# Performance work log

Hardware: AMD Instinct MI355X
Metric: run time of the kernel (lower is better)

## Reference

```python
import jax, jax.numpy as jnp
import numpy as np

B, C_IN, C, H, W = 32, 2048, 1024, 14, 14
N_CLS = 30


def setup_inputs() -> dict:
    key = jax.random.key(0)
    k1, k2, k3, k4, k5 = jax.random.split(key, 5)
    f1 = jax.random.normal(k1, (B, C_IN, H, W), dtype=jnp.float32)
    f2 = jax.random.normal(k2, (B, C, H, W), dtype=jnp.float32)
    conv_w = jax.random.normal(k3, (C, C_IN), dtype=jnp.float32) * (1.0 / np.sqrt(C_IN))
    fc_w = jax.random.normal(k4, (N_CLS, C), dtype=jnp.float32) * (1.0 / np.sqrt(C))
    fc_b = jax.random.normal(k5, (N_CLS,), dtype=jnp.float32)
    return {"f1": f1, "f2": f2, "conv_w": conv_w, "fc_w": fc_w, "fc_b": fc_b}


def reference(f1, f2, conv_w, fc_w, fc_b):
    # conv1: 1x1 conv 2048 -> 1024, no bias  => channel contraction
    f1c = jnp.einsum('bihw,oi->bohw', f1, conv_w)  # [B, C, H, W]

    # bilinear_pooling: out[b,c,h,i,j] = f1c[b,c,h,i] * f2[b,c,h,j]
    # followed by AdaptiveAvgPool2d((1,1)) over (H, W*W).
    # mean_{h,i,j} f1c*f2 = mean_h[ (mean_i f1c) * (mean_j f2) ]
    xm = jnp.mean(f1c, axis=-1)              # [B, C, H]
    ym = jnp.mean(f2, axis=-1)               # [B, C, H]
    pooled = jnp.mean(xm * ym, axis=-1)      # [B, C]

    # fc head
    return pooled @ fc_w.T + fc_b            # [B, 30]
```

## Files before the change

### kernel.cpp

```cpp
#include <hip/hip_runtime.h>
#include <hip/hip_bf16.h>


typedef __attribute__((ext_vector_type(8))) short short8;
typedef __attribute__((ext_vector_type(4))) float f32x4;

static __device__ __forceinline__ unsigned short f2bf(float f) {
    union { float f; unsigned u; } v; v.f = f;
    return (unsigned short)((v.u + 0x7FFFu + ((v.u >> 16) & 1u)) >> 16);
}

__global__ __launch_bounds__(256) void k1_prep(
    const float* __restrict__ f1, const float* __restrict__ f2,
    const float* __restrict__ cw,
    unsigned short* __restrict__ f1mt, unsigned short* __restrict__ cwb,
    float* __restrict__ ym)
{
    __shared__ float lds[64 * 196];
    const float inv14 = 1.0f / 14.0f;
    int blk = blockIdx.x;
    int tid = threadIdx.x;

    if (blk < 1024) {
        int b = blk >> 5, i0 = (blk & 31) * 64;
        const float4* src = (const float4*)(f1 + (size_t)(b * 2048 + i0) * 196);
        #pragma unroll
        for (int j = 0; j < 13; j++) {
            int idx = j * 256 + tid;
            if (idx < 3136) *(float4*)&lds[idx * 4] = src[idx];
        }
        __syncthreads();
        int r  = tid & 63;
        int hb = tid >> 6;
        unsigned short* o = f1mt + (size_t)b * 16 * 2048 + i0 + r;
        #pragma unroll
        for (int it = 0; it < 4; it++) {
            int h = hb + it * 4;
            if (h < 14) {
                const float* p = &lds[r * 196 + h * 14];
                float s = 0.0f;
                #pragma unroll
                for (int q = 0; q < 14; q++) s += p[q];
                o[h * 2048] = f2bf(s * inv14);
            } else {
                o[h * 2048] = 0;
            }
        }
    } else if (blk < 1536) {
        int t = blk - 1024;
        int b = t >> 4, c0 = (t & 15) * 64;
        const float4* src = (const float4*)(f2 + (size_t)(b * 1024 + c0) * 196);
        #pragma unroll
        for (int j = 0; j < 13; j++) {
            int idx = j * 256 + tid;
            if (idx < 3136) *(float4*)&lds[idx * 4] = src[idx];
        }
        __syncthreads();
        int r  = tid & 63;
        int hb = tid >> 6;
        float* o = ym + (size_t)b * 16 * 1024 + c0 + r;
        #pragma unroll
        for (int it = 0; it < 4; it++) {
            int h = hb + it * 4;
            if (h < 14) {
                const float* p = &lds[r * 196 + h * 14];
                float s = 0.0f;
                #pragma unroll
                for (int q = 0; q < 14; q++) s += p[q];
                o[h * 1024] = s * inv14;
            } else {
                o[h * 1024] = 0.0f;
            }
        }
    } else {
        int t = (blk - 1536) * 256 + tid;
        const float4* p = (const float4*)(cw + (size_t)t * 8);
        float4 v0 = p[0], v1 = p[1];
        ushort4 a, b4;
        a.x = f2bf(v0.x); a.y = f2bf(v0.y); a.z = f2bf(v0.z); a.w = f2bf(v0.w);
        b4.x = f2bf(v1.x); b4.y = f2bf(v1.y); b4.z = f2bf(v1.z); b4.w = f2bf(v1.w);
        *(ushort4*)(cwb + (size_t)t * 8)     = a;
        *(ushort4*)(cwb + (size_t)t * 8 + 4) = b4;
    }
}

__global__ __launch_bounds__(256) void k2_gemm(
    const unsigned short* __restrict__ A,
    const unsigned short* __restrict__ Bm,
    const float* __restrict__ ym,
    float* __restrict__ part)
{
    int tid = threadIdx.x;
    int w  = tid >> 6;
    int l  = tid & 63;
    int lg = l >> 4;
    int lr = l & 15;
    int tile = blockIdx.x >> 2;
    int kq   = blockIdx.x & 3;
    int ct = tile >> 3, nt = tile & 7;
    int c0 = ct * 64, n0 = nt * 64;
    int kc = kq * 4 + w;
    int kbase = kc * 128;

    const unsigned short* Ap = A  + (size_t)(c0 + lr) * 2048 + kbase + lg * 8;
    const unsigned short* Bp = Bm + (size_t)(n0 + lr) * 2048 + kbase + lg * 8;

    short8 af[4][4], bf[4][4];
    #pragma unroll
    for (int mf = 0; mf < 4; mf++)
        #pragma unroll
        for (int kk = 0; kk < 4; kk++)
            af[mf][kk] = *(const short8*)(Ap + mf * 16 * 2048 + kk * 32);
    #pragma unroll
    for (int nf = 0; nf < 4; nf++)
        #pragma unroll
        for (int kk = 0; kk < 4; kk++)
            bf[nf][kk] = *(const short8*)(Bp + nf * 16 * 2048 + kk * 32);

    f32x4 acc[4][4];
    #pragma unroll
    for (int mf = 0; mf < 4; mf++)
        #pragma unroll
        for (int nf = 0; nf < 4; nf++)
            acc[mf][nf] = (f32x4){0.f, 0.f, 0.f, 0.f};

    #pragma unroll
    for (int kk = 0; kk < 4; kk++)
        #pragma unroll
        for (int mf = 0; mf < 4; mf++)
            #pragma unroll
            for (int nf = 0; nf < 4; nf++)
                acc[mf][nf] = __builtin_amdgcn_mfma_f32_16x16x32_bf16(
                    af[mf][kk], bf[nf][kk], acc[mf][nf], 0, 0, 0);

    const float inv14 = 1.0f / 14.0f;
    #pragma unroll
    for (int nf = 0; nf < 4; nf++) {
        int b = nt * 4 + nf;
        const float* yrow = ym + (size_t)(b * 16 + lr) * 1024 + c0 + lg * 4;
        #pragma unroll
        for (int mf = 0; mf < 4; mf++) {
            f32x4 yv = *(const f32x4*)(yrow + mf * 16);
            f32x4 pp = acc[mf][nf] * yv;
            #pragma unroll
            for (int st = 1; st <= 8; st <<= 1) {
                pp[0] += __shfl_xor(pp[0], st);
                pp[1] += __shfl_xor(pp[1], st);
                pp[2] += __shfl_xor(pp[2], st);
                pp[3] += __shfl_xor(pp[3], st);
            }
            if (lr == 0) {
                float* dst = part + (size_t)kc * 32768 + b * 1024 + c0 + mf * 16 + lg * 4;
                *(f32x4*)dst = pp * inv14;
            }
        }
    }
}

__global__ __launch_bounds__(256) void k3_fc(
    const float* __restrict__ part, const float* __restrict__ fcw,
    const float* __restrict__ fcb, float* __restrict__ out)
{
    __shared__ float ps[1024];
    int b = blockIdx.x, tid = threadIdx.x;
    #pragma unroll
    for (int c = tid; c < 1024; c += 256) {
        float s = 0.0f;
        #pragma unroll
        for (int k = 0; k < 16; k++)
            s += part[(size_t)k * 32768 + b * 1024 + c];
        ps[c] = s;
    }
    __syncthreads();
    int w = tid >> 6, l = tid & 63;
    const float4* pp = (const float4*)ps;
    for (int n = w; n < 30; n += 4) {
        const float4* wp = (const float4*)(fcw + n * 1024);
        float s = 0.0f;
        #pragma unroll
        for (int it = 0; it < 4; it++) {
            float4 wv = wp[l + it * 64];
            float4 pv = pp[l + it * 64];
            s += wv.x * pv.x + wv.y * pv.y + wv.z * pv.z + wv.w * pv.w;
        }
        #pragma unroll
        for (int m = 32; m; m >>= 1) s += __shfl_xor(s, m);
        if (l == 0) out[b * 30 + n] = s + fcb[n];
    }
}

extern "C" void kernel_launch(void* const* d_in, const int* in_sizes, int n_in,
                              void* d_out, int out_size, void* d_ws, size_t ws_size,
                              hipStream_t stream) {
    const float* f1  = (const float*)d_in[0];
    const float* f2  = (const float*)d_in[1];
    const float* cw  = (const float*)d_in[2];
    const float* fcw = (const float*)d_in[3];
    const float* fcb = (const float*)d_in[4];
    float* out = (float*)d_out;

    unsigned short* f1mt = (unsigned short*)d_ws;
    unsigned short* cwb  = (unsigned short*)((char*)d_ws + (2u << 20));
    float* ym            = (float*)((char*)d_ws + (6u << 20));
    float* part          = (float*)((char*)d_ws + (8u << 20));

    k1_prep<<<2560, 256, 0, stream>>>(f1, f2, cw, f1mt, cwb, ym);
    k2_gemm<<<512, 256, 0, stream>>>(cwb, f1mt, ym, part);
    k3_fc<<<32, 256, 0, stream>>>(part, fcw, fcb, out);
}
```

Before: 136.6 us.

## Pad LDS rows, shrink GEMM tiles with XCD swizzle, widen FC block

The prep kernel pads each LDS row to 197 floats so the per-row strided reads land in different banks. The GEMM kernel halves the N tile to 32, doubles the grid to 1024 blocks and remaps block IDs so neighbouring tiles fall on the same XCD. It also splits the K loads into two halves to cut register pressure. The FC kernel runs with 1024 threads so each thread reduces one channel. Padding makes the LDS float4 stores misaligned, and the smaller tiles load each A fragment more times.

```diff
diff --git a/kernel.cpp b/kernel.cpp
--- a/kernel.cpp
+++ b/kernel.cpp
@@ -9,6 +9,8 @@
     union { float f; unsigned u; } v; v.f = f;
     return (unsigned short)((v.u + 0x7FFFu + ((v.u >> 16) & 1u)) >> 16);
 }
+
+#define LROW 197
 
 __global__ __launch_bounds__(256) void k1_prep(
     const float* __restrict__ f1, const float* __restrict__ f2,
@@ -16,7 +18,7 @@
     unsigned short* __restrict__ f1mt, unsigned short* __restrict__ cwb,
     float* __restrict__ ym)
 {
-    __shared__ float lds[64 * 196];
+    __shared__ float lds[64 * LROW];
     const float inv14 = 1.0f / 14.0f;
     int blk = blockIdx.x;
     int tid = threadIdx.x;
@@ -26,8 +28,11 @@
         const float4* src = (const float4*)(f1 + (size_t)(b * 2048 + i0) * 196);
         #pragma unroll
         for (int j = 0; j < 13; j++) {
-            int idx = j * 256 + tid;
-            if (idx < 3136) *(float4*)&lds[idx * 4] = src[idx];
+            unsigned idx = j * 256 + tid;
+            if (idx < 3136) {
+                unsigned row = idx / 49, col = idx - row * 49;
+                *(float4*)&lds[row * LROW + col * 4] = src[idx];
+            }
         }
         __syncthreads();
         int r  = tid & 63;
@@ -37,7 +42,7 @@
         for (int it = 0; it < 4; it++) {
             int h = hb + it * 4;
             if (h < 14) {
-                const float* p = &lds[r * 196 + h * 14];
+                const float* p = &lds[r * LROW + h * 14];
                 float s = 0.0f;
                 #pragma unroll
                 for (int q = 0; q < 14; q++) s += p[q];
@@ -52,8 +57,11 @@
         const float4* src = (const float4*)(f2 + (size_t)(b * 1024 + c0) * 196);
         #pragma unroll
         for (int j = 0; j < 13; j++) {
-            int idx = j * 256 + tid;
-            if (idx < 3136) *(float4*)&lds[idx * 4] = src[idx];
+            unsigned idx = j * 256 + tid;
+            if (idx < 3136) {
+                unsigned row = idx / 49, col = idx - row * 49;
+                *(float4*)&lds[row * LROW + col * 4] = src[idx];
+            }
         }
         __syncthreads();
         int r  = tid & 63;
@@ -63,7 +71,7 @@
         for (int it = 0; it < 4; it++) {
             int h = hb + it * 4;
             if (h < 14) {
-                const float* p = &lds[r * 196 + h * 14];
+                const float* p = &lds[r * LROW + h * 14];
                 float s = 0.0f;
                 #pragma unroll
                 for (int q = 0; q < 14; q++) s += p[q];
@@ -95,48 +103,54 @@
     int l  = tid & 63;
     int lg = l >> 4;
     int lr = l & 15;
-    int tile = blockIdx.x >> 2;
-    int kq   = blockIdx.x & 3;
-    int ct = tile >> 3, nt = tile & 7;
-    int c0 = ct * 64, n0 = nt * 64;
+
+    int bid = blockIdx.x;
+    int sid = (bid & 7) * 128 + (bid >> 3);
+    int ct  = sid >> 6;
+    int rem = sid & 63;
+    int nt  = rem >> 2;
+    int kq  = rem & 3;
+    int c0 = ct * 64, n0 = nt * 32;
     int kc = kq * 4 + w;
     int kbase = kc * 128;
 
     const unsigned short* Ap = A  + (size_t)(c0 + lr) * 2048 + kbase + lg * 8;
     const unsigned short* Bp = Bm + (size_t)(n0 + lr) * 2048 + kbase + lg * 8;
 
-    short8 af[4][4], bf[4][4];
+    f32x4 acc[4][2];
     #pragma unroll
     for (int mf = 0; mf < 4; mf++)
         #pragma unroll
-        for (int kk = 0; kk < 4; kk++)
-            af[mf][kk] = *(const short8*)(Ap + mf * 16 * 2048 + kk * 32);
-    #pragma unroll
-    for (int nf = 0; nf < 4; nf++)
-        #pragma unroll
-        for (int kk = 0; kk < 4; kk++)
-            bf[nf][kk] = *(const short8*)(Bp + nf * 16 * 2048 + kk * 32);
-
-    f32x4 acc[4][4];
-    #pragma unroll
-    for (int mf = 0; mf < 4; mf++)
-        #pragma unroll
-        for (int nf = 0; nf < 4; nf++)
+        for (int nf = 0; nf < 2; nf++)
             acc[mf][nf] = (f32x4){0.f, 0.f, 0.f, 0.f};
 
-    #pragma unroll
-    for (int kk = 0; kk < 4; kk++)
-        #pragma unroll
-        for (int mf = 0; mf < 4; mf++)
-            #pragma unroll
-            for (int nf = 0; nf < 4; nf++)
-                acc[mf][nf] = __builtin_amdgcn_mfma_f32_16x16x32_bf16(
-                    af[mf][kk], bf[nf][kk], acc[mf][nf], 0, 0, 0);
+    #pragma unroll 1
+    for (int half = 0; half < 2; half++) {
+        short8 af[4][2], bf[2][2];
+        #pragma unroll
+        for (int kk = 0; kk < 2; kk++) {
+            int ko = half * 64 + kk * 32;
+            #pragma unroll
+            for (int mf = 0; mf < 4; mf++)
+                af[mf][kk] = *(const short8*)(Ap + mf * 16 * 2048 + ko);
+            #pragma unroll
+            for (int nf = 0; nf < 2; nf++)
+                bf[nf][kk] = *(const short8*)(Bp + nf * 16 * 2048 + ko);
+        }
+        #pragma unroll
+        for (int kk = 0; kk < 2; kk++)
+            #pragma unroll
+            for (int mf = 0; mf < 4; mf++)
+                #pragma unroll
+                for (int nf = 0; nf < 2; nf++)
+                    acc[mf][nf] = __builtin_amdgcn_mfma_f32_16x16x32_bf16(
+                        af[mf][kk], bf[nf][kk], acc[mf][nf], 0, 0, 0);
+    }
 
     const float inv14 = 1.0f / 14.0f;
     #pragma unroll
-    for (int nf = 0; nf < 4; nf++) {
-        int b = nt * 4 + nf;
+    for (int nf = 0; nf < 2; nf++) {
+        int b = nt * 2 + nf;
         const float* yrow = ym + (size_t)(b * 16 + lr) * 1024 + c0 + lg * 4;
         #pragma unroll
         for (int mf = 0; mf < 4; mf++) {
@@ -157,35 +171,28 @@
     }
 }
 
-__global__ __launch_bounds__(256) void k3_fc(
+__global__ __launch_bounds__(1024) void k3_fc(
     const float* __restrict__ part, const float* __restrict__ fcw,
     const float* __restrict__ fcb, float* __restrict__ out)
 {
     __shared__ float ps[1024];
     int b = blockIdx.x, tid = threadIdx.x;
+    float s = 0.0f;
     #pragma unroll
-    for (int c = tid; c < 1024; c += 256) {
-        float s = 0.0f;
-        #pragma unroll
-        for (int k = 0; k < 16; k++)
-            s += part[(size_t)k * 32768 + b * 1024 + c];
-        ps[c] = s;
-    }
+    for (int k = 0; k < 16; k++)
+        s += part[(size_t)k * 32768 + b * 1024 + tid];
+    ps[tid] = s;
     __syncthreads();
     int w = tid >> 6, l = tid & 63;
-    const float4* pp = (const float4*)ps;
-    for (int n = w; n < 30; n += 4) {
-        const float4* wp = (const float4*)(fcw + n * 1024);
-        float s = 0.0f;
-        #pragma unroll
-        for (int it = 0; it < 4; it++) {
-            float4 wv = wp[l + it * 64];
-            float4 pv = pp[l + it * 64];
-            s += wv.x * pv.x + wv.y * pv.y + wv.z * pv.z + wv.w * pv.w;
-        }
-        #pragma unroll
-        for (int m = 32; m; m >>= 1) s += __shfl_xor(s, m);
-        if (l == 0) out[b * 30 + n] = s + fcb[n];
+    for (int n = w; n < 30; n += 16) {
+        const float* wp = fcw + n * 1024;
+        float t = 0.0f;
+        #pragma unroll
+        for (int it = 0; it < 16; it++)
+            t += wp[l + it * 64] * ps[l + it * 64];
+        #pragma unroll
+        for (int m = 32; m; m >>= 1) t += __shfl_xor(t, m);
+        if (l == 0) out[b * 30 + n] = t + fcb[n];
     }
 }
 
@@ -205,6 +212,6 @@
     float* part          = (float*)((char*)d_ws + (8u << 20));
 
     k1_prep<<<2560, 256, 0, stream>>>(f1, f2, cw, f1mt, cwb, ym);
-    k2_gemm<<<512, 256, 0, stream>>>(cwb, f1mt, ym, part);
-    k3_fc<<<32, 256, 0, stream>>>(part, fcw, fcb, out);
-}
+    k2_gemm<<<1024, 256, 0, stream>>>(cwb, f1mt, ym, part);
+    k3_fc<<<32, 1024, 0, stream>>>(part, fcw, fcb, out);
+}
```

New measurement: 133.9 us. 2.0% less time.
